# Optimization experiments

Measured on AMD Instinct MI355X. Metric: run time of the kernel, lower is better.

## Reference

```python
import jax, jax.numpy as jnp
import numpy as np

N = 50000      # nodes
E = 800000     # edges (before self loops)
IN = 256       # in_dim
HID = 32       # hidden_dim per head
H = 8          # heads layer 1
OUT = 64       # out_dim (classes)
NEG_SLOPE = 0.2  # PyG GATConv default


def gat_conv(x, ei, W, a_src, a_dst, b, heads, ch, concat):
    """PyG GATConv (eval mode, self-loops already in ei).
    x: [n, f_in], ei: [2, e] (row0=src j, row1=dst i), W: [f_in, heads*ch],
    a_src/a_dst: [heads, ch], b: [heads*ch] or [ch]."""
    n = x.shape[0]
    h = (x @ W).reshape(n, heads, ch)                      # [n, H, C]
    src, dst = ei[0], ei[1]
    alpha_src = (h * a_src).sum(-1)                        # [n, H]
    alpha_dst = (h * a_dst).sum(-1)                        # [n, H]
    e = jax.nn.leaky_relu(alpha_src[src] + alpha_dst[dst], NEG_SLOPE)  # [e, H]
    # segment softmax over incoming edges of each dst node
    emax = jax.lax.stop_gradient(jax.ops.segment_max(e, dst, num_segments=n))
    p = jnp.exp(e - emax[dst])
    denom = jax.ops.segment_sum(p, dst, num_segments=n)    # [n, H] (>0: self loops)
    alpha = p / denom[dst]                                 # [e, H]
    out = jax.ops.segment_sum(h[src] * alpha[:, :, None], dst, num_segments=n)  # [n, H, C]
    out = out.reshape(n, heads * ch) if concat else out.mean(axis=1)
    return out + b


def setup_inputs() -> dict:
    key = jax.random.key(0)
    ks = jax.random.split(key, 9)
    x = jax.random.normal(ks[0], (N, IN), jnp.float32)
    edge_index = jax.random.randint(ks[1], (2, E), 0, N, jnp.int32)
    W1 = jax.random.normal(ks[2], (IN, H * HID), jnp.float32) * 0.05
    a_src1 = jax.random.normal(ks[3], (H, HID), jnp.float32) * 0.1
    a_dst1 = jax.random.normal(ks[4], (H, HID), jnp.float32) * 0.1
    b1 = jnp.zeros((H * HID,), jnp.float32)
    W2 = jax.random.normal(ks[5], (H * HID, OUT), jnp.float32) * 0.05
    a_src2 = jax.random.normal(ks[6], (1, OUT), jnp.float32) * 0.1
    a_dst2 = jax.random.normal(ks[7], (1, OUT), jnp.float32) * 0.1
    b2 = jnp.zeros((OUT,), jnp.float32)
    return {"x": x, "edge_index": edge_index, "W1": W1, "a_src1": a_src1,
            "a_dst1": a_dst1, "b1": b1, "W2": W2, "a_src2": a_src2,
            "a_dst2": a_dst2, "b2": b2}


def reference(x, edge_index, W1, a_src1, a_dst1, b1, W2, a_src2, a_dst2, b2):
    n = x.shape[0]
    loops = jnp.arange(n, dtype=edge_index.dtype)
    ei = jnp.concatenate([edge_index, jnp.stack([loops, loops])], axis=1)  # add self loops
    h = gat_conv(x, ei, W1, a_src1, a_dst1, b1, H, HID, concat=True)
    h = jax.nn.relu(h)
    h = gat_conv(h, ei, W2, a_src2, a_dst2, b2, 1, OUT, concat=False)
    return jax.nn.log_softmax(h, axis=1)
```

## Files before the change

kernel.cpp:

```cpp
#include <hip/hip_runtime.h>
#include <math.h>

#define NNODES 50000
#define EORIG  800000
#define ETOT   850000
#define NBUCK  196
#define BSTRIDE 5120
#define P2CHUNK 4096
#define NBLK2  ((ETOT + P2CHUNK - 1)/P2CHUNK)

typedef __attribute__((ext_vector_type(8))) short bf8_t;
typedef __attribute__((ext_vector_type(4))) float f4_t;
typedef __attribute__((ext_vector_type(2))) float f2_t;

constexpr float LOG2E = 1.44269504f;

constexpr size_t align256(size_t x){ return (x + 255) & ~size_t(255); }
constexpr size_t OFF_OFFSETS = 0;
constexpr size_t OFF_DEG     = OFF_OFFSETS + align256((size_t)NNODES*4);
constexpr size_t OFF_GCUR    = OFF_DEG     + align256((size_t)NNODES*4);
constexpr size_t OFF_EPACK   = OFF_GCUR    + align256(NBUCK*4);
constexpr size_t OFF_SRC     = OFF_EPACK   + align256((size_t)NBUCK*BSTRIDE*4);
constexpr size_t OFF_AS1     = OFF_SRC     + align256((size_t)NBUCK*BSTRIDE*4);
constexpr size_t OFF_AD1     = OFF_AS1     + align256((size_t)NNODES*8*4);
constexpr size_t OFF_W1T     = OFF_AD1     + align256((size_t)NNODES*8*4);
constexpr size_t OFF_W2T     = OFF_W1T     + align256(256*256*2);
constexpr size_t OFF_H1F8    = OFF_W2T     + align256(64*256*2);
constexpr size_t OFF_OUT1B   = OFF_H1F8    + align256((size_t)NNODES*256);
constexpr size_t OFF_H2B     = OFF_H1F8;
constexpr size_t OFF_AS2     = OFF_OUT1B   + align256((size_t)NNODES*256*2);
constexpr size_t OFF_AD2     = OFF_AS2     + align256((size_t)NNODES*4);

__device__ __forceinline__ unsigned short f2bf(float f){
    union { float f; unsigned u; } v; v.f = f;
    unsigned r = v.u + 0x7FFF + ((v.u >> 16) & 1);
    return (unsigned short)(r >> 16);
}
__device__ __forceinline__ float bf2f(unsigned short s){
    union { unsigned u; float f; } v; v.u = ((unsigned)s) << 16;
    return v.f;
}


__global__ __launch_bounds__(256) void p3_part(const int* __restrict__ ei, int* __restrict__ gcur,
                                               int* __restrict__ epack){
    __shared__ int h[NBUCK];
    __shared__ int r[NBUCK];
    const int t = threadIdx.x;
    for (int i = t; i < NBUCK; i += 256){ h[i] = 0; r[i] = 0; }
    __syncthreads();
    const int base = blockIdx.x * P2CHUNK;
    int srcs[P2CHUNK/256], dsts[P2CHUNK/256];
#pragma unroll
    for (int j = 0; j < P2CHUNK/256; j++){
        int e = base + j*256 + t;
        if (e < ETOT){
            if (e < EORIG){ srcs[j] = ei[e]; dsts[j] = ei[EORIG + e]; }
            else          { srcs[j] = dsts[j] = e - EORIG; }
            atomicAdd(&h[dsts[j] >> 8], 1);
        } else dsts[j] = -1;
    }
    __syncthreads();
    for (int i = t; i < NBUCK; i += 256){
        int c = h[i];
        h[i] = c ? atomicAdd(&gcur[i], c) : 0;
    }
    __syncthreads();
#pragma unroll
    for (int j = 0; j < P2CHUNK/256; j++){
        if (dsts[j] >= 0){
            int b = dsts[j] >> 8;
            int rk = atomicAdd(&r[b], 1);
            epack[h[b] + rk] = (srcs[j] << 8) | (dsts[j] & 255);
        }
    }
}

__global__ __launch_bounds__(256) void p4_csr(const int* __restrict__ gcur, const int* __restrict__ epack,
                                              int* __restrict__ offsets, int* __restrict__ deg_g,
                                              int* __restrict__ srclist){
    __shared__ int deg[256];
    __shared__ int sm[256];
    __shared__ int cur[256];
    const int b = blockIdx.x, t = threadIdx.x;
    const int s0 = b * BSTRIDE, s1 = gcur[b];
    deg[t] = 0; __syncthreads();
    for (int i = s0 + t; i < s1; i += 256) atomicAdd(&deg[epack[i] & 255], 1);
    __syncthreads();
    int v = deg[t];
    sm[t] = v; __syncthreads();
    for (int off = 1; off < 256; off <<= 1){
        int add = (t >= off) ? sm[t-off] : 0;
        __syncthreads();
        sm[t] += add;
        __syncthreads();
    }
    int excl = sm[t] - v;
    int node = (b << 8) + t;
    if (node < NNODES){ offsets[node] = s0 + excl; deg_g[node] = v; }
    cur[t] = s0 + excl;
    __syncthreads();
    for (int i = s0 + t; i < s1; i += 256){
        int p = epack[i];
        int pos = atomicAdd(&cur[p & 255], 1);
        srclist[pos] = p >> 8;
    }
}


__global__ __launch_bounds__(256) void conv_w_k(const float* __restrict__ W1, const float* __restrict__ W2,
                                                short* __restrict__ w1t, short* __restrict__ w2t,
                                                int* __restrict__ gcur){
    int o = blockIdx.x*256 + threadIdx.x;
    if (o < NBUCK) gcur[o] = o * BSTRIDE;
    if (o < 256*256){
        int n = o >> 8, k = o & 255;
        w1t[o] = (short)f2bf(W1[k*256 + n]);
    } else {
        int o2 = o - 256*256;
        if (o2 < 64*256){
            int n = o2 >> 8, k = o2 & 255;
            w2t[o2] = (short)f2bf(W2[k*64 + n]);
        }
    }
}


__global__ __launch_bounds__(256) void gemm1_mfma(const float* __restrict__ x, const short* __restrict__ w1t,
        const float* __restrict__ a1s, const float* __restrict__ a1d,
        unsigned char* __restrict__ h1f8, float* __restrict__ as1, float* __restrict__ ad1){
    __shared__ short As[2][64][40];
    const int t = threadIdx.x;
    const int lane = t & 63, wave = t >> 6;
    const int quad = lane >> 4, l15 = lane & 15;
    const int r0 = blockIdx.x * 64;
    const int srow = t >> 2, skoff = (t & 3) * 8;
    const bool arow_ok = (r0 + srow) < NNODES;
    const float* xrow = x + (size_t)(r0 + srow)*256 + skoff;
    const short* wbase = w1t + (size_t)(wave*64 + l15)*256 + quad*8;
    f4_t zero4 = {0.f,0.f,0.f,0.f};
    f4_t acc[4][4];
#pragma unroll
    for (int i=0;i<4;i++)
#pragma unroll
      for (int j=0;j<4;j++) acc[i][j] = zero4;

    float4 xa0 = {0,0,0,0}, xa1 = {0,0,0,0};
    if (arow_ok){ xa0 = *(const float4*)(xrow); xa1 = *(const float4*)(xrow + 4); }
    bf8_t bcur[4], bnxt[4];
#pragma unroll
    for (int j=0;j<4;j++) bcur[j] = *(const bf8_t*)(wbase + j*16*256);
    {
        bf8_t a0;
        a0[0]=f2bf(xa0.x); a0[1]=f2bf(xa0.y); a0[2]=f2bf(xa0.z); a0[3]=f2bf(xa0.w);
        a0[4]=f2bf(xa1.x); a0[5]=f2bf(xa1.y); a0[6]=f2bf(xa1.z); a0[7]=f2bf(xa1.w);
        *(bf8_t*)&As[0][srow][skoff] = a0;
    }
    __syncthreads();
    int cur = 0;
#pragma unroll
    for (int s = 0; s < 8; s++){
        if (s < 7){
            const int kn = s*32 + 32;
            if (arow_ok){ xa0 = *(const float4*)(xrow + kn); xa1 = *(const float4*)(xrow + kn + 4); }
#pragma unroll
            for (int j=0;j<4;j++) bnxt[j] = *(const bf8_t*)(wbase + j*16*256 + kn);
        }
        bf8_t af[4];
#pragma unroll
        for (int i=0;i<4;i++) af[i] = *(const bf8_t*)&As[cur][i*16 + l15][quad*8];
#pragma unroll
        for (int i=0;i<4;i++)
#pragma unroll
          for (int j=0;j<4;j++)
            acc[i][j] = __builtin_amdgcn_mfma_f32_16x16x32_bf16(af[i], bcur[j], acc[i][j], 0,0,0);
        if (s < 7){
            bf8_t a0;
            a0[0]=f2bf(xa0.x); a0[1]=f2bf(xa0.y); a0[2]=f2bf(xa0.z); a0[3]=f2bf(xa0.w);
            a0[4]=f2bf(xa1.x); a0[5]=f2bf(xa1.y); a0[6]=f2bf(xa1.z); a0[7]=f2bf(xa1.w);
            *(bf8_t*)&As[cur^1][srow][skoff] = a0;
            __syncthreads();
            cur ^= 1;
#pragma unroll
            for (int j=0;j<4;j++) bcur[j] = bnxt[j];
        }
    }
    const int colbase = wave*64;
    const int head0 = colbase >> 5;
    float cs[4], cd[4];
#pragma unroll
    for (int j=0;j<4;j++){
        cs[j] = a1s[colbase + j*16 + l15] * LOG2E;
        cd[j] = a1d[colbase + j*16 + l15] * LOG2E;
    }
#pragma unroll
    for (int i=0;i<4;i++){
        int rowb = r0 + i*16 + quad*4;
#pragma unroll
        for (int reg=0; reg<4; reg++){
            int row = rowb + reg;
            bool valid = row < NNODES;
            float sp0=0.f, dp0=0.f, sp1=0.f, dp1=0.f;
#pragma unroll
            for (int j=0;j<4;j++){
                float v = acc[i][j][reg];
                if (j < 2){ sp0 += v*cs[j]; dp0 += v*cd[j]; }
                else      { sp1 += v*cs[j]; dp1 += v*cd[j]; }
                if (valid){
                    unsigned enc = (unsigned)__builtin_amdgcn_cvt_pk_fp8_f32(v, v, 0, false);
                    h1f8[(size_t)row*256 + colbase + j*16 + l15] = (unsigned char)(enc & 0xffu);
                }
            }
            sp0 += __shfl_xor(sp0,1); sp0 += __shfl_xor(sp0,2); sp0 += __shfl_xor(sp0,4); sp0 += __shfl_xor(sp0,8);
            dp0 += __shfl_xor(dp0,1); dp0 += __shfl_xor(dp0,2); dp0 += __shfl_xor(dp0,4); dp0 += __shfl_xor(dp0,8);
            sp1 += __shfl_xor(sp1,1); sp1 += __shfl_xor(sp1,2); sp1 += __shfl_xor(sp1,4); sp1 += __shfl_xor(sp1,8);
            dp1 += __shfl_xor(dp1,1); dp1 += __shfl_xor(dp1,2); dp1 += __shfl_xor(dp1,4); dp1 += __shfl_xor(dp1,8);
            if (valid && l15 == 0){
                as1[row*8 + head0    ] = sp0;
                ad1[row*8 + head0    ] = dp0;
                as1[row*8 + head0 + 1] = sp1;
                ad1[row*8 + head0 + 1] = dp1;
            }
        }
    }
}


__global__ __launch_bounds__(256) void gemm2_mfma(const short* __restrict__ ab, const short* __restrict__ w2t,
        const float* __restrict__ a2s, const float* __restrict__ a2d,
        short* __restrict__ h2b, float* __restrict__ as2, float* __restrict__ ad2){
    __shared__ short As[2][64][40];
    const int t = threadIdx.x;
    const int lane = t & 63, wave = t >> 6;
    const int quad = lane >> 4, l15 = lane & 15;
    const int r0 = blockIdx.x * 64;
    const int srow = t >> 2, skoff = (t & 3) * 8;
    const bool arow_ok = (r0 + srow) < NNODES;
    const short* arow = ab + (size_t)(r0 + srow)*256 + skoff;
    const short* wbase = w2t + (size_t)l15*256 + quad*8;
    f4_t zero4 = {0.f,0.f,0.f,0.f};
    f4_t acc[4];
#pragma unroll
    for (int j=0;j<4;j++) acc[j] = zero4;

    bf8_t a0 = {};
    if (arow_ok) a0 = *(const bf8_t*)(arow);
    bf8_t bcur[4], bnxt[4];
#pragma unroll
    for (int j=0;j<4;j++) bcur[j] = *(const bf8_t*)(wbase + j*16*256);
    *(bf8_t*)&As[0][srow][skoff] = a0;
    __syncthreads();
    int cur = 0;
#pragma unroll
    for (int s = 0; s < 8; s++){
        bf8_t anx = {};
        if (s < 7){
            const int kn = s*32 + 32;
            if (arow_ok) anx = *(const bf8_t*)(arow + kn);
#pragma unroll
            for (int j=0;j<4;j++) bnxt[j] = *(const bf8_t*)(wbase + j*16*256 + kn);
        }
        bf8_t af = *(const bf8_t*)&As[cur][wave*16 + l15][quad*8];
#pragma unroll
        for (int j=0;j<4;j++)
            acc[j] = __builtin_amdgcn_mfma_f32_16x16x32_bf16(af, bcur[j], acc[j], 0,0,0);
        if (s < 7){
            *(bf8_t*)&As[cur^1][srow][skoff] = anx;
            __syncthreads();
            cur ^= 1;
#pragma unroll
            for (int j=0;j<4;j++) bcur[j] = bnxt[j];
        }
    }
    float cs[4], cd[4];
#pragma unroll
    for (int j=0;j<4;j++){
        cs[j] = a2s[j*16 + l15] * LOG2E;
        cd[j] = a2d[j*16 + l15] * LOG2E;
    }
    int rowb = r0 + wave*16 + quad*4;
#pragma unroll
    for (int reg=0; reg<4; reg++){
        int row = rowb + reg;
        bool valid = row < NNODES;
        float sp=0.f, dp=0.f;
#pragma unroll
        for (int j=0;j<4;j++){
            float v = acc[j][reg];
            sp += v*cs[j]; dp += v*cd[j];
            if (valid) h2b[(size_t)row*64 + j*16 + l15] = (short)f2bf(v);
        }
        sp += __shfl_xor(sp,1); sp += __shfl_xor(sp,2); sp += __shfl_xor(sp,4); sp += __shfl_xor(sp,8);
        dp += __shfl_xor(dp,1); dp += __shfl_xor(dp,2); dp += __shfl_xor(dp,4); dp += __shfl_xor(dp,8);
        if (valid && l15 == 0){ as2[row] = sp; ad2[row] = dp; }
    }
}


__global__ __launch_bounds__(256) void aggregate1_k(const unsigned char* __restrict__ h1f8,
        const float* __restrict__ as1, const float* __restrict__ ad1,
        const int* __restrict__ offsets, const int* __restrict__ deg_g,
        const int* __restrict__ srclist,
        const float* __restrict__ b1, short* __restrict__ out1b){
    int d = blockIdx.x*4 + (threadIdx.x >> 6);
    int lane = threadIdx.x & 63;
    if (d >= NNODES) return;
    const int sub    = lane >> 4;
    const int c16    = lane & 15;
    const int head_g = c16 >> 1;
    const int head_p = lane & 7;
    const int ep     = lane >> 3;
    int start = offsets[d];
    int deg = deg_g[d];
    float ad_p = ad1[d*8 + head_p];
    float denom = 0.f;
    f2_t acc[8];
#pragma unroll
    for (int i=0;i<8;i++) acc[i] = (f2_t){0.f,0.f};
    for (int w = 0; w < deg; w += 64){
        int deg_w = min(64, deg - w);
        int s_reg = srclist[start + w + min(lane, deg_w-1)];
        int ngr = (deg_w + 7) >> 3;
        auto comp_p = [&](int g)->float{
            int ei = g*8 + ep;
            int s  = __shfl(s_reg, min(ei, deg_w-1));
            float e = as1[s*8 + head_p] + ad_p;
            e = fmaxf(0.2f*e, e);
            float p = exp2f(e);
            return (ei < deg_w) ? p : 0.f;
        };
        float p_reg = comp_p(0);
        for (int g = 0; g < ngr; g++){
            float p_cur = p_reg;
            if (g + 1 < ngr) p_reg = comp_p(g+1);
#pragma unroll
            for (int q = 0; q < 2; q++){
                int eq = q*4 + sub;
                float pe = __shfl(p_cur, eq*8 + head_g);
                int   se = __shfl(s_reg, g*8 + eq);
                uint4 wv = *(const uint4*)(h1f8 + (size_t)se*256 + c16*16);
                f2_t v;
                v = __builtin_amdgcn_cvt_pk_f32_fp8(wv.x, false); acc[0] += pe*v;
                v = __builtin_amdgcn_cvt_pk_f32_fp8(wv.x, true);  acc[1] += pe*v;
                v = __builtin_amdgcn_cvt_pk_f32_fp8(wv.y, false); acc[2] += pe*v;
                v = __builtin_amdgcn_cvt_pk_f32_fp8(wv.y, true);  acc[3] += pe*v;
                v = __builtin_amdgcn_cvt_pk_f32_fp8(wv.z, false); acc[4] += pe*v;
                v = __builtin_amdgcn_cvt_pk_f32_fp8(wv.z, true);  acc[5] += pe*v;
                v = __builtin_amdgcn_cvt_pk_f32_fp8(wv.w, false); acc[6] += pe*v;
                v = __builtin_amdgcn_cvt_pk_f32_fp8(wv.w, true);  acc[7] += pe*v;
                denom += pe;
            }
        }
    }
#pragma unroll
    for (int i=0;i<8;i++){
        acc[i][0] += __shfl_xor(acc[i][0], 16);
        acc[i][1] += __shfl_xor(acc[i][1], 16);
        acc[i][0] += __shfl_xor(acc[i][0], 32);
        acc[i][1] += __shfl_xor(acc[i][1], 32);
    }
    denom += __shfl_xor(denom, 16);
    denom += __shfl_xor(denom, 32);
    if (sub == 0){
        float inv = 1.f / denom;
        const float4 bv0 = *(const float4*)(b1 + c16*16);
        const float4 bv1 = *(const float4*)(b1 + c16*16 + 4);
        const float4 bv2 = *(const float4*)(b1 + c16*16 + 8);
        const float4 bv3 = *(const float4*)(b1 + c16*16 + 12);
        bf8_t r0, r1;
        r0[0] = (short)f2bf(fmaxf(acc[0][0]*inv + bv0.x, 0.f));
        r0[1] = (short)f2bf(fmaxf(acc[0][1]*inv + bv0.y, 0.f));
        r0[2] = (short)f2bf(fmaxf(acc[1][0]*inv + bv0.z, 0.f));
        r0[3] = (short)f2bf(fmaxf(acc[1][1]*inv + bv0.w, 0.f));
        r0[4] = (short)f2bf(fmaxf(acc[2][0]*inv + bv1.x, 0.f));
        r0[5] = (short)f2bf(fmaxf(acc[2][1]*inv + bv1.y, 0.f));
        r0[6] = (short)f2bf(fmaxf(acc[3][0]*inv + bv1.z, 0.f));
        r0[7] = (short)f2bf(fmaxf(acc[3][1]*inv + bv1.w, 0.f));
        r1[0] = (short)f2bf(fmaxf(acc[4][0]*inv + bv2.x, 0.f));
        r1[1] = (short)f2bf(fmaxf(acc[4][1]*inv + bv2.y, 0.f));
        r1[2] = (short)f2bf(fmaxf(acc[5][0]*inv + bv2.z, 0.f));
        r1[3] = (short)f2bf(fmaxf(acc[5][1]*inv + bv2.w, 0.f));
        r1[4] = (short)f2bf(fmaxf(acc[6][0]*inv + bv3.x, 0.f));
        r1[5] = (short)f2bf(fmaxf(acc[6][1]*inv + bv3.y, 0.f));
        r1[6] = (short)f2bf(fmaxf(acc[7][0]*inv + bv3.z, 0.f));
        r1[7] = (short)f2bf(fmaxf(acc[7][1]*inv + bv3.w, 0.f));
        *(bf8_t*)(out1b + (size_t)d*256 + c16*16)     = r0;
        *(bf8_t*)(out1b + (size_t)d*256 + c16*16 + 8) = r1;
    }
}

__global__ __launch_bounds__(256) void aggregate2_k(const unsigned short* __restrict__ h2b,
        const float* __restrict__ as2, const float* __restrict__ ad2,
        const int* __restrict__ offsets, const int* __restrict__ deg_g,
        const int* __restrict__ srclist,
        const float* __restrict__ b2, float* __restrict__ out){
    int d = blockIdx.x*4 + (threadIdx.x >> 6);
    int lane = threadIdx.x & 63;
    if (d >= NNODES) return;
    const int sub = lane >> 3;
    const int c8  = lane & 7;
    int start = offsets[d];
    int deg = deg_g[d];
    float ad_v = ad2[d];
    float denom = 0.f;
    float accv[8] = {0.f,0.f,0.f,0.f,0.f,0.f,0.f,0.f};
    for (int w = 0; w < deg; w += 64){
        int deg_w = min(64, deg - w);
        int s_reg = srclist[start + w + min(lane, deg_w-1)];
        float ev = as2[s_reg] + ad_v;
        ev = fmaxf(0.2f*ev, ev);
        float p_lane = (lane < deg_w) ? exp2f(ev) : 0.f;
        int ngr = (deg_w + 7) >> 3;
        for (int g = 0; g < ngr; g++){
            int eq = g*8 + sub;
            float pe = __shfl(p_lane, eq);
            int   se = __shfl(s_reg, eq);
            bf8_t hv = *(const bf8_t*)(h2b + (size_t)se*64 + c8*8);
#pragma unroll
            for (int k=0;k<8;k++) accv[k] += pe * bf2f((unsigned short)hv[k]);
            denom += pe;
        }
    }
#pragma unroll
    for (int k=0;k<8;k++){
        accv[k] += __shfl_xor(accv[k], 8);
        accv[k] += __shfl_xor(accv[k], 16);
        accv[k] += __shfl_xor(accv[k], 32);
    }
    denom += __shfl_xor(denom, 8);
    denom += __shfl_xor(denom, 16);
    denom += __shfl_xor(denom, 32);
    float inv = 1.f / denom;
    float v[8];
    float mx = -1e30f;
#pragma unroll
    for (int k=0;k<8;k++){
        v[k] = accv[k]*inv + b2[c8*8 + k];
        mx = fmaxf(mx, v[k]);
    }
    mx = fmaxf(mx, __shfl_xor(mx, 1));
    mx = fmaxf(mx, __shfl_xor(mx, 2));
    mx = fmaxf(mx, __shfl_xor(mx, 4));
    float ss = 0.f;
#pragma unroll
    for (int k=0;k<8;k++) ss += __expf(v[k] - mx);
    ss += __shfl_xor(ss, 1);
    ss += __shfl_xor(ss, 2);
    ss += __shfl_xor(ss, 4);
    if (sub == 0){
        float lg = mx + __logf(ss);
        float4 o0 = {v[0]-lg, v[1]-lg, v[2]-lg, v[3]-lg};
        float4 o1 = {v[4]-lg, v[5]-lg, v[6]-lg, v[7]-lg};
        *(float4*)(out + (size_t)d*64 + c8*8)     = o0;
        *(float4*)(out + (size_t)d*64 + c8*8 + 4) = o1;
    }
}


extern "C" void kernel_launch(void* const* d_in, const int* in_sizes, int n_in,
                              void* d_out, int out_size, void* d_ws, size_t ws_size,
                              hipStream_t stream){
    const float* x      = (const float*)d_in[0];
    const int*   ei     = (const int*)  d_in[1];
    const float* W1     = (const float*)d_in[2];
    const float* a_src1 = (const float*)d_in[3];
    const float* a_dst1 = (const float*)d_in[4];
    const float* b1     = (const float*)d_in[5];
    const float* W2     = (const float*)d_in[6];
    const float* a_src2 = (const float*)d_in[7];
    const float* a_dst2 = (const float*)d_in[8];
    const float* b2     = (const float*)d_in[9];

    char* ws = (char*)d_ws;
    int*   offsets = (int*)  (ws + OFF_OFFSETS);
    int*   deg_g   = (int*)  (ws + OFF_DEG);
    int*   gcur    = (int*)  (ws + OFF_GCUR);
    int*   epack   = (int*)  (ws + OFF_EPACK);
    int*   srclist = (int*)  (ws + OFF_SRC);
    float* as1     = (float*)(ws + OFF_AS1);
    float* ad1     = (float*)(ws + OFF_AD1);
    short* w1t     = (short*)(ws + OFF_W1T);
    short* w2t     = (short*)(ws + OFF_W2T);
    unsigned char* h1f8 = (unsigned char*)(ws + OFF_H1F8);
    short* out1b   = (short*)(ws + OFF_OUT1B);
    short* h2b     = (short*)(ws + OFF_H2B);
    float* as2     = (float*)(ws + OFF_AS2);
    float* ad2     = (float*)(ws + OFF_AD2);

    conv_w_k<<<(256*256 + 64*256 + 255)/256, 256, 0, stream>>>(W1, W2, w1t, w2t, gcur);

    p3_part<<<NBLK2, 256, 0, stream>>>(ei, gcur, epack);
    p4_csr <<<NBUCK, 256, 0, stream>>>(gcur, epack, offsets, deg_g, srclist);

    gemm1_mfma<<<(NNODES+63)/64, 256, 0, stream>>>(x, w1t, a_src1, a_dst1, h1f8, as1, ad1);
    aggregate1_k<<<(NNODES+3)/4, 256, 0, stream>>>(h1f8, as1, ad1, offsets, deg_g, srclist, b1, out1b);

    gemm2_mfma<<<(NNODES+63)/64, 256, 0, stream>>>(out1b, w2t, a_src2, a_dst2, h2b, as2, ad2);
    aggregate2_k<<<(NNODES+3)/4, 256, 0, stream>>>((const unsigned short*)h2b, as2, ad2, offsets, deg_g, srclist, b2, (float*)d_out);
}
```

Before: 257.6 us.

## Store layer-1 features head-major and aggregate one head per block

Layer-1 fp8 features and attention-source/destination scores are written in a head-major layout by gemm1. The first aggregation launches one block group per head, so each wave gathers only a 32-byte slice of a single head's feature table. The intent is to shrink the working set of the random gathers so it stays cache-resident. The trade-off is eight times more blocks, each re-reading the CSR offsets and source lists and recomputing per-edge softmax weights, plus narrower per-lane loads.

```diff
diff --git a/kernel.cpp b/kernel.cpp
--- a/kernel.cpp
+++ b/kernel.cpp
@@ -208,7 +208,8 @@
                 else      { sp1 += v*cs[j]; dp1 += v*cd[j]; }
                 if (valid){
                     unsigned enc = (unsigned)__builtin_amdgcn_cvt_pk_fp8_f32(v, v, 0, false);
-                    h1f8[(size_t)row*256 + colbase + j*16 + l15] = (unsigned char)(enc & 0xffu);
+                    int col = colbase + j*16 + l15;
+                    h1f8[((size_t)(col >> 5)*NNODES + row)*32 + (col & 31)] = (unsigned char)(enc & 0xffu);
                 }
             }
             sp0 += __shfl_xor(sp0,1); sp0 += __shfl_xor(sp0,2); sp0 += __shfl_xor(sp0,4); sp0 += __shfl_xor(sp0,8);
@@ -216,10 +217,10 @@
             sp1 += __shfl_xor(sp1,1); sp1 += __shfl_xor(sp1,2); sp1 += __shfl_xor(sp1,4); sp1 += __shfl_xor(sp1,8);
             dp1 += __shfl_xor(dp1,1); dp1 += __shfl_xor(dp1,2); dp1 += __shfl_xor(dp1,4); dp1 += __shfl_xor(dp1,8);
             if (valid && l15 == 0){
-                as1[row*8 + head0    ] = sp0;
-                ad1[row*8 + head0    ] = dp0;
-                as1[row*8 + head0 + 1] = sp1;
-                ad1[row*8 + head0 + 1] = dp1;
+                as1[(size_t) head0   *NNODES + row] = sp0;
+                ad1[(size_t) head0   *NNODES + row] = dp0;
+                as1[(size_t)(head0+1)*NNODES + row] = sp1;
+                ad1[(size_t)(head0+1)*NNODES + row] = dp1;
             }
         }
     }
@@ -302,90 +303,57 @@
         const int* __restrict__ offsets, const int* __restrict__ deg_g,
         const int* __restrict__ srclist,
         const float* __restrict__ b1, short* __restrict__ out1b){
-    int d = blockIdx.x*4 + (threadIdx.x >> 6);
+    const int bid  = blockIdx.x;
+    const int head = bid & 7;
+    int d = (bid >> 3)*4 + (threadIdx.x >> 6);
     int lane = threadIdx.x & 63;
     if (d >= NNODES) return;
-    const int sub    = lane >> 4;
-    const int c16    = lane & 15;
-    const int head_g = c16 >> 1;
-    const int head_p = lane & 7;
-    const int ep     = lane >> 3;
+    const int es = lane >> 3;
+    const int cl = lane & 7;
+    const unsigned char* __restrict__ hs  = h1f8 + (size_t)head*NNODES*32;
+    const float* __restrict__ ass = as1 + (size_t)head*NNODES;
     int start = offsets[d];
     int deg = deg_g[d];
-    float ad_p = ad1[d*8 + head_p];
+    float ad_h = ad1[(size_t)head*NNODES + d];
     float denom = 0.f;
-    f2_t acc[8];
-#pragma unroll
-    for (int i=0;i<8;i++) acc[i] = (f2_t){0.f,0.f};
+    f2_t a01 = {0.f,0.f}, a23 = {0.f,0.f};
     for (int w = 0; w < deg; w += 64){
         int deg_w = min(64, deg - w);
         int s_reg = srclist[start + w + min(lane, deg_w-1)];
+        float e = ass[s_reg] + ad_h;
+        e = fmaxf(0.2f*e, e);
+        float p_lane = (lane < deg_w) ? exp2f(e) : 0.f;
         int ngr = (deg_w + 7) >> 3;
-        auto comp_p = [&](int g)->float{
-            int ei = g*8 + ep;
-            int s  = __shfl(s_reg, min(ei, deg_w-1));
-            float e = as1[s*8 + head_p] + ad_p;
-            e = fmaxf(0.2f*e, e);
-            float p = exp2f(e);
-            return (ei < deg_w) ? p : 0.f;
-        };
-        float p_reg = comp_p(0);
         for (int g = 0; g < ngr; g++){
-            float p_cur = p_reg;
-            if (g + 1 < ngr) p_reg = comp_p(g+1);
-#pragma unroll
-            for (int q = 0; q < 2; q++){
-                int eq = q*4 + sub;
-                float pe = __shfl(p_cur, eq*8 + head_g);
-                int   se = __shfl(s_reg, g*8 + eq);
-                uint4 wv = *(const uint4*)(h1f8 + (size_t)se*256 + c16*16);
-                f2_t v;
-                v = __builtin_amdgcn_cvt_pk_f32_fp8(wv.x, false); acc[0] += pe*v;
-                v = __builtin_amdgcn_cvt_pk_f32_fp8(wv.x, true);  acc[1] += pe*v;
-                v = __builtin_amdgcn_cvt_pk_f32_fp8(wv.y, false); acc[2] += pe*v;
-                v = __builtin_amdgcn_cvt_pk_f32_fp8(wv.y, true);  acc[3] += pe*v;
-                v = __builtin_amdgcn_cvt_pk_f32_fp8(wv.z, false); acc[4] += pe*v;
-                v = __builtin_amdgcn_cvt_pk_f32_fp8(wv.z, true);  acc[5] += pe*v;
-                v = __builtin_amdgcn_cvt_pk_f32_fp8(wv.w, false); acc[6] += pe*v;
-                v = __builtin_amdgcn_cvt_pk_f32_fp8(wv.w, true);  acc[7] += pe*v;
-                denom += pe;
-            }
-        }
-    }
-#pragma unroll
-    for (int i=0;i<8;i++){
-        acc[i][0] += __shfl_xor(acc[i][0], 16);
-        acc[i][1] += __shfl_xor(acc[i][1], 16);
-        acc[i][0] += __shfl_xor(acc[i][0], 32);
-        acc[i][1] += __shfl_xor(acc[i][1], 32);
-    }
-    denom += __shfl_xor(denom, 16);
-    denom += __shfl_xor(denom, 32);
-    if (sub == 0){
+            int ee = g*8 + es;
+            float pe = __shfl(p_lane, ee);
+            int   se = __shfl(s_reg, ee);
+            unsigned wv = *(const unsigned*)(hs + (size_t)se*32 + cl*4);
+            f2_t lo = __builtin_amdgcn_cvt_pk_f32_fp8(wv, false);
+            f2_t hi = __builtin_amdgcn_cvt_pk_f32_fp8(wv, true);
+            a01 += pe*lo;
+            a23 += pe*hi;
+            denom += pe;
+        }
+    }
+    a01[0] += __shfl_xor(a01[0], 8);  a01[1] += __shfl_xor(a01[1], 8);
+    a23[0] += __shfl_xor(a23[0], 8);  a23[1] += __shfl_xor(a23[1], 8);
+    denom  += __shfl_xor(denom, 8);
+    a01[0] += __shfl_xor(a01[0], 16); a01[1] += __shfl_xor(a01[1], 16);
+    a23[0] += __shfl_xor(a23[0], 16); a23[1] += __shfl_xor(a23[1], 16);
+    denom  += __shfl_xor(denom, 16);
+    a01[0] += __shfl_xor(a01[0], 32); a01[1] += __shfl_xor(a01[1], 32);
+    a23[0] += __shfl_xor(a23[0], 32); a23[1] += __shfl_xor(a23[1], 32);
+    denom  += __shfl_xor(denom, 32);
+    if (es == 0){
         float inv = 1.f / denom;
-        const float4 bv0 = *(const float4*)(b1 + c16*16);
-        const float4 bv1 = *(const float4*)(b1 + c16*16 + 4);
-        const float4 bv2 = *(const float4*)(b1 + c16*16 + 8);
-        const float4 bv3 = *(const float4*)(b1 + c16*16 + 12);
-        bf8_t r0, r1;
-        r0[0] = (short)f2bf(fmaxf(acc[0][0]*inv + bv0.x, 0.f));
-        r0[1] = (short)f2bf(fmaxf(acc[0][1]*inv + bv0.y, 0.f));
-        r0[2] = (short)f2bf(fmaxf(acc[1][0]*inv + bv0.z, 0.f));
-        r0[3] = (short)f2bf(fmaxf(acc[1][1]*inv + bv0.w, 0.f));
-        r0[4] = (short)f2bf(fmaxf(acc[2][0]*inv + bv1.x, 0.f));
-        r0[5] = (short)f2bf(fmaxf(acc[2][1]*inv + bv1.y, 0.f));
-        r0[6] = (short)f2bf(fmaxf(acc[3][0]*inv + bv1.z, 0.f));
-        r0[7] = (short)f2bf(fmaxf(acc[3][1]*inv + bv1.w, 0.f));
-        r1[0] = (short)f2bf(fmaxf(acc[4][0]*inv + bv2.x, 0.f));
-        r1[1] = (short)f2bf(fmaxf(acc[4][1]*inv + bv2.y, 0.f));
-        r1[2] = (short)f2bf(fmaxf(acc[5][0]*inv + bv2.z, 0.f));
-        r1[3] = (short)f2bf(fmaxf(acc[5][1]*inv + bv2.w, 0.f));
-        r1[4] = (short)f2bf(fmaxf(acc[6][0]*inv + bv3.x, 0.f));
-        r1[5] = (short)f2bf(fmaxf(acc[6][1]*inv + bv3.y, 0.f));
-        r1[6] = (short)f2bf(fmaxf(acc[7][0]*inv + bv3.z, 0.f));
-        r1[7] = (short)f2bf(fmaxf(acc[7][1]*inv + bv3.w, 0.f));
-        *(bf8_t*)(out1b + (size_t)d*256 + c16*16)     = r0;
-        *(bf8_t*)(out1b + (size_t)d*256 + c16*16 + 8) = r1;
+        const float4 bv = *(const float4*)(b1 + head*32 + cl*4);
+        ushort4 us;
+        us.x = f2bf(fmaxf(a01[0]*inv + bv.x, 0.f));
+        us.y = f2bf(fmaxf(a01[1]*inv + bv.y, 0.f));
+        us.z = f2bf(fmaxf(a23[0]*inv + bv.z, 0.f));
+        us.w = f2bf(fmaxf(a23[1]*inv + bv.w, 0.f));
+        *(ushort4*)(out1b + (size_t)d*256 + head*32 + cl*4) = us;
     }
 }
 
@@ -493,7 +461,7 @@
     p4_csr <<<NBUCK, 256, 0, stream>>>(gcur, epack, offsets, deg_g, srclist);
 
     gemm1_mfma<<<(NNODES+63)/64, 256, 0, stream>>>(x, w1t, a_src1, a_dst1, h1f8, as1, ad1);
-    aggregate1_k<<<(NNODES+3)/4, 256, 0, stream>>>(h1f8, as1, ad1, offsets, deg_g, srclist, b1, out1b);
+    aggregate1_k<<<((NNODES+3)/4)*8, 256, 0, stream>>>(h1f8, as1, ad1, offsets, deg_g, srclist, b1, out1b);
 
     gemm2_mfma<<<(NNODES+63)/64, 256, 0, stream>>>(out1b, w2t, a_src2, a_dst2, h2b, as2, ad2);
     aggregate2_k<<<(NNODES+3)/4, 256, 0, stream>>>((const unsigned short*)h2b, as2, ad2, offsets, deg_g, srclist, b2, (float*)d_out);
```

New measurement: 344.2 us. 33.6% more time.
